# Kernel optimization log

Measured on AMD Instinct MI355X. Metric: run time of the kernel, lower is better.

The kernel has to match this reference:

```python
import jax, jax.numpy as jnp
import numpy as np

N = 200000      # total nodes
E = 800000      # directed edges
G = 4096        # graphs in batch
D_DRUG = 128
D_CELL = 954
HID = 128
OUT = 128
EPS = 1e-5      # BatchNorm eps


def _bn(x, gamma, beta):
    # training-mode BatchNorm1d (batch statistics, biased var), dropout is eval/identity
    m = jnp.mean(x, axis=0)
    v = jnp.mean((x - m) ** 2, axis=0)
    return gamma * (x - m) * jax.lax.rsqrt(v + EPS) + beta


def _gcn_conv(x, edge_index, W, b):
    # PyG GCNConv: add self-loops, symmetric normalization, aggregate, then bias
    src = jnp.concatenate([edge_index[0], jnp.arange(N)])
    dst = jnp.concatenate([edge_index[1], jnp.arange(N)])
    ones = jnp.ones(src.shape[0], dtype=x.dtype)
    deg = jax.ops.segment_sum(ones, dst, num_segments=N)
    dinv = jnp.where(deg > 0, jax.lax.rsqrt(jnp.maximum(deg, 1.0)), 0.0)
    norm = dinv[src] * dinv[dst]                      # [E+N]
    h = x @ W                                         # [N, out]
    msg = h[src] * norm[:, None]                      # gather + scale
    out = jax.ops.segment_sum(msg, dst, num_segments=N)  # scatter-add
    return out + b


def setup_inputs() -> dict:
    key = jax.random.key(0)
    ks = jax.random.split(key, 12)
    x = jax.random.normal(ks[0], (N, D_DRUG), jnp.float32)
    edge_index = jax.random.randint(ks[1], (2, E), 0, N)
    ibatch = (jnp.arange(N) * G) // N  # sorted, every graph non-empty
    gexpr = jax.random.normal(ks[2], (G, D_CELL), jnp.float32)

    def w(k, shape):
        return jax.random.normal(k, shape, jnp.float32) / np.float32(np.sqrt(shape[0]))

    return {
        "x": x, "edge_index": edge_index, "ibatch": ibatch, "gexpr": gexpr,
        "W1": w(ks[3], (D_DRUG, HID)), "b1": jnp.zeros((HID,), jnp.float32),
        "g1": jnp.ones((HID,), jnp.float32), "be1": jnp.zeros((HID,), jnp.float32),
        "W2": w(ks[4], (HID, OUT)), "b2": jnp.zeros((OUT,), jnp.float32),
        "g2": jnp.ones((OUT,), jnp.float32), "be2": jnp.zeros((OUT,), jnp.float32),
        "Wc1": w(ks[5], (D_CELL, HID)), "bc1": jnp.zeros((HID,), jnp.float32),
        "gc": jnp.ones((HID,), jnp.float32), "bec": jnp.zeros((HID,), jnp.float32),
        "Wc2": w(ks[6], (HID, OUT)), "bc2": jnp.zeros((OUT,), jnp.float32),
    }


def reference(x, edge_index, ibatch, gexpr,
              W1, b1, g1, be1, W2, b2, g2, be2,
              Wc1, bc1, gc, bec, Wc2, bc2):
    # drug branch
    h = _gcn_conv(x, edge_index, W1, b1)
    h = _bn(jax.nn.relu(h), g1, be1)
    h = _gcn_conv(h, edge_index, W2, b2)
    h = _bn(jax.nn.relu(h), g2, be2)
    x_drug = jax.ops.segment_max(h, ibatch, num_segments=G)  # global_max_pool
    # cellline branch
    c = jnp.tanh(gexpr @ Wc1 + bc1)
    c = _bn(c, gc, bec)
    x_cell = jax.nn.relu(c @ Wc2 + bc2)
    return x_drug, x_cell
```

## Files before the change

### kernel.cpp

```cpp
#include <hip/hip_runtime.h>

#define NFEAT 128

typedef __attribute__((ext_vector_type(4))) float f32x4;
typedef __attribute__((ext_vector_type(8))) short bf16x8;

__device__ __forceinline__ unsigned short f2bf(float f) {
    unsigned u = __builtin_bit_cast(unsigned, f);
    u += 0x7fffu + ((u >> 16) & 1u);
    return (unsigned short)(u >> 16);
}
__device__ __forceinline__ float bf2f(unsigned short s) {
    unsigned u = ((unsigned)s) << 16;
    return __builtin_bit_cast(float, u);
}

__device__ __forceinline__ void dma16(const void* g, void* l) {
    __builtin_amdgcn_global_load_lds(
        (const __attribute__((address_space(1))) unsigned int*)g,
        (__attribute__((address_space(3))) unsigned int*)l, 16, 0, 0);
}

template <int ACT, typename OutT, typename AT>
__global__ __launch_bounds__(256) void gemm_dma(
    const AT* __restrict__ A, const unsigned short* __restrict__ Bt,
    OutT* __restrict__ C, int M, int ldA, int ldB,
    const float* __restrict__ bias, const float* __restrict__ dscale)
{
    constexpr bool AF32 = (sizeof(AT) == 4);
    __shared__ AT ash[64 * 128];
    const int tid = threadIdx.x;
    const int wv = tid >> 6, lane = tid & 63;
    const int l16 = lane & 15, quad = lane >> 4;
    const int kbase = blockIdx.y * 128;
    const long tile0 = (long)blockIdx.x * 64;

    const int nc0 = (wv & 1) * 64;
    bf16x8 bfr[4][4];
#pragma unroll
    for (int nt = 0; nt < 4; ++nt) {
        const unsigned short* bp =
            Bt + (size_t)(nc0 + nt * 16 + l16) * ldB + kbase + quad * 8;
#pragma unroll
        for (int ks = 0; ks < 4; ++ks)
            bfr[nt][ks] = *(const bf16x8*)(bp + ks * 32);
    }

    {
        const int r0 = wv * 16;
        if constexpr (AF32) {
#pragma unroll
            for (int j = 0; j < 8; ++j) {
                const float* gp = (const float*)A +
                    (size_t)(tile0 + r0 + j * 2 + (lane >> 5)) * ldA + kbase +
                    (lane & 31) * 4;
                dma16(gp, (void*)&ash[(r0 + j * 2) * 128]);
            }
        } else {
#pragma unroll
            for (int j = 0; j < 4; ++j) {
                const unsigned short* gp = (const unsigned short*)A +
                    (size_t)(tile0 + r0 + j * 4 + (lane >> 4)) * ldA + kbase +
                    l16 * 8;
                dma16(gp, (void*)&ash[(r0 + j * 4) * 128]);
            }
        }
    }
    __syncthreads();

    const int rh = wv >> 1;
    bf16x8 af[2][4];
#pragma unroll
    for (int mt = 0; mt < 2; ++mt) {
        const int row = rh * 32 + mt * 16 + l16;
#pragma unroll
        for (int ks = 0; ks < 4; ++ks) {
            if constexpr (AF32) {
                const float* lp = (const float*)&ash[0] + row * 128 + ks * 32 + quad * 8;
                f32x4 v0 = *(const f32x4*)lp;
                f32x4 v1 = *(const f32x4*)(lp + 4);
                bf16x8 t;
                t[0] = (short)f2bf(v0[0]); t[1] = (short)f2bf(v0[1]);
                t[2] = (short)f2bf(v0[2]); t[3] = (short)f2bf(v0[3]);
                t[4] = (short)f2bf(v1[0]); t[5] = (short)f2bf(v1[1]);
                t[6] = (short)f2bf(v1[2]); t[7] = (short)f2bf(v1[3]);
                af[mt][ks] = t;
            } else {
                af[mt][ks] = *(const bf16x8*)((const unsigned short*)&ash[0] +
                                              row * 128 + ks * 32 + quad * 8);
            }
        }
    }

    f32x4 acc[2][4];
#pragma unroll
    for (int a = 0; a < 2; ++a)
#pragma unroll
        for (int b = 0; b < 4; ++b) acc[a][b] = (f32x4){0.f, 0.f, 0.f, 0.f};
#pragma unroll
    for (int ks = 0; ks < 4; ++ks)
#pragma unroll
        for (int nt = 0; nt < 4; ++nt)
#pragma unroll
            for (int mt = 0; mt < 2; ++mt)
                acc[mt][nt] = __builtin_amdgcn_mfma_f32_16x16x32_bf16(
                    af[mt][ks], bfr[nt][ks], acc[mt][nt], 0, 0, 0);

    C += (size_t)blockIdx.y * M * NFEAT;
    float ds[2][4];
#pragma unroll
    for (int mt = 0; mt < 2; ++mt)
#pragma unroll
        for (int r = 0; r < 4; ++r) {
            long row = tile0 + rh * 32 + mt * 16 + quad * 4 + r;
            ds[mt][r] = dscale ? dscale[row] : 1.f;
        }
#pragma unroll
    for (int nt = 0; nt < 4; ++nt) {
        int col = nc0 + nt * 16 + l16;
        float bv = bias ? bias[col] : 0.f;
#pragma unroll
        for (int mt = 0; mt < 2; ++mt) {
            long rbase = tile0 + rh * 32 + mt * 16 + quad * 4;
#pragma unroll
            for (int r = 0; r < 4; ++r) {
                float v = acc[mt][nt][r] + bv;
                if (ACT == 1) v = tanhf(v);
                if (ACT == 2) v = fmaxf(v, 0.f);
                v *= ds[mt][r];
                if constexpr (sizeof(OutT) == 2)
                    C[(size_t)(rbase + r) * NFEAT + col] = (OutT)f2bf(v);
                else
                    C[(size_t)(rbase + r) * NFEAT + col] = (OutT)v;
            }
        }
    }
}

__global__ void k_transpose(const float* __restrict__ W, unsigned short* __restrict__ Wt,
                            int K, int Kp)
{
    int idx = blockIdx.x * 256 + threadIdx.x;
    if (idx >= 128 * Kp) return;
    int n = idx / Kp, k = idx - n * Kp;
    Wt[idx] = (k < K) ? f2bf(W[(size_t)k * NFEAT + n]) : (unsigned short)0;
}

__global__ void k_bnfold_w(const float* __restrict__ sums8, const float* __restrict__ gamma,
                           const float* __restrict__ beta, float invN,
                           const float* __restrict__ W, const float* __restrict__ extra,
                           unsigned short* __restrict__ Wt, float* __restrict__ brow)
{
    __shared__ float ssc[128], ssh[128];
    int t = threadIdx.x;
    if (t < 128) {
        float s = 0.f, s2 = 0.f;
#pragma unroll
        for (int c = 0; c < 8; ++c) { s += sums8[c * 256 + t]; s2 += sums8[c * 256 + 128 + t]; }
        float mean = s * invN;
        float var = s2 * invN - mean * mean;
        float rstd = rsqrtf(fmaxf(var, 0.f) + 1e-5f);
        float sc = gamma[t] * rstd;
        ssc[t] = sc;
        ssh[t] = beta[t] - mean * sc;
    }
    __syncthreads();
    if (blockIdx.x < 64) {
        int idx = blockIdx.x * 256 + t;
        int n = idx >> 7, k = idx & 127;
        Wt[idx] = f2bf(W[(size_t)k * NFEAT + n] * ssc[k]);
    } else if (t < 128) {
        float s = extra ? extra[t] : 0.f;
        for (int k = 0; k < 128; ++k) s += ssh[k] * W[(size_t)k * NFEAT + t];
        brow[t] = s;
    }
}

__global__ void k_finalize8(const float* __restrict__ sums8, const float* __restrict__ gamma,
                            const float* __restrict__ beta, float* __restrict__ scale,
                            float* __restrict__ shift, float invN)
{
    int j = threadIdx.x;
    float s = 0.f, s2 = 0.f;
#pragma unroll
    for (int c = 0; c < 8; ++c) { s += sums8[c * 256 + j]; s2 += sums8[c * 256 + 128 + j]; }
    float mean = s * invN;
    float var = s2 * invN - mean * mean;
    float rstd = rsqrtf(fmaxf(var, 0.f) + 1e-5f);
    float sc = gamma[j] * rstd;
    scale[j] = sc;
    shift[j] = beta[j] - mean * sc;
}

__global__ void k_padA(const float* __restrict__ g, float* __restrict__ Ap,
                       int G, int DC, int DCP)
{
    long idx = (long)blockIdx.x * 256 + threadIdx.x;
    if (idx >= (long)G * DCP) return;
    long i = idx / DCP; int k = (int)(idx - i * DCP);
    Ap[idx] = (k < DC) ? g[i * DC + k] : 0.f;
}

__global__ void k_degi(const int* __restrict__ dst, int* __restrict__ deg, int E)
{
    int e = blockIdx.x * 256 + threadIdx.x;
    if (e < E) atomicAdd(&deg[dst[e]], 1);
}

__global__ __launch_bounds__(256) void k_scan1(const int* __restrict__ deg,
        int* __restrict__ rowptr, int* __restrict__ bsum, float* __restrict__ dinv, int N)
{
    __shared__ int sh[256];
    int t = threadIdx.x;
    int base = blockIdx.x * 1024 + t * 4;
    int v[4];
#pragma unroll
    for (int j = 0; j < 4; ++j) {
        v[j] = (base + j < N) ? deg[base + j] : 0;
        if (base + j < N) dinv[base + j] = rsqrtf((float)(v[j] + 1));
    }
    int s = v[0] + v[1] + v[2] + v[3];
    sh[t] = s;
    __syncthreads();
    int incl = s;
    for (int off = 1; off < 256; off <<= 1) {
        int x = (t >= off) ? sh[t - off] : 0;
        __syncthreads();
        incl += x;
        sh[t] = incl;
        __syncthreads();
    }
    int run = incl - s;
#pragma unroll
    for (int j = 0; j < 4; ++j) {
        if (base + j < N) rowptr[base + j] = run;
        run += v[j];
    }
    if (t == 255) bsum[blockIdx.x] = incl;
}

__global__ void k_scan2(int* __restrict__ bsum, int nb)
{
    __shared__ int sh[256];
    int t = threadIdx.x;
    int s = (t < nb) ? bsum[t] : 0;
    sh[t] = s;
    __syncthreads();
    int incl = s;
    for (int off = 1; off < 256; off <<= 1) {
        int x = (t >= off) ? sh[t - off] : 0;
        __syncthreads();
        incl += x;
        sh[t] = incl;
        __syncthreads();
    }
    if (t < nb) bsum[t] = incl - s;
}

__global__ void k_scan3(int* __restrict__ rowptr, int* __restrict__ cursor,
                        const int* __restrict__ bsum, int N, int E)
{
    int i = blockIdx.x * 256 + threadIdx.x;
    if (i < N) {
        int v = rowptr[i] + bsum[i >> 10];
        rowptr[i] = v;
        cursor[i] = v;
    } else if (i == N) {
        rowptr[N] = E;
    }
}

__global__ void k_fill(const int* __restrict__ src, const int* __restrict__ dst,
                       int* __restrict__ cursor, int* __restrict__ csr, int E)
{
    int e = blockIdx.x * 256 + threadIdx.x;
    if (e < E) {
        int pos = atomicAdd(&cursor[dst[e]], 1);
        csr[pos] = src[e];
    }
}

__device__ __forceinline__ void unpack_add(float* acc, uint4 a)
{
    acc[0] += bf2f((unsigned short)(a.x & 0xffff));
    acc[1] += bf2f((unsigned short)(a.x >> 16));
    acc[2] += bf2f((unsigned short)(a.y & 0xffff));
    acc[3] += bf2f((unsigned short)(a.y >> 16));
    acc[4] += bf2f((unsigned short)(a.z & 0xffff));
    acc[5] += bf2f((unsigned short)(a.z >> 16));
    acc[6] += bf2f((unsigned short)(a.w & 0xffff));
    acc[7] += bf2f((unsigned short)(a.w >> 16));
}

__device__ __forceinline__ void row_gather(const unsigned short* __restrict__ h,
    const int* __restrict__ rowptr, const int* __restrict__ csr,
    long i, int f, int N, float* acc)
{
    int lo = rowptr[i], hi = rowptr[i + 1];
    int n = hi - lo;
    int idx[6];
#pragma unroll
    for (int j = 0; j < 6; ++j) {
        int cv = csr[lo + j];
        idx[j] = (j < n) ? cv : N;
    }
    uint4 ga[6];
#pragma unroll
    for (int j = 0; j < 6; ++j)
        ga[j] = *(const uint4*)(h + ((size_t)idx[j] << 7) + f);
    uint4 gs = *(const uint4*)(h + ((size_t)i << 7) + f);
#pragma unroll
    for (int j = 0; j < 6; ++j) unpack_add(acc, ga[j]);
    unpack_add(acc, gs);
    if (n > 6) {
        int e = lo + 6;
        for (; e + 1 < hi; e += 2) {
            uint4 a = *(const uint4*)(h + ((size_t)csr[e] << 7) + f);
            uint4 b = *(const uint4*)(h + ((size_t)csr[e + 1] << 7) + f);
            unpack_add(acc, a); unpack_add(acc, b);
        }
        if (e < hi) {
            uint4 a = *(const uint4*)(h + ((size_t)csr[e] << 7) + f);
            unpack_add(acc, a);
        }
    }
}

__global__ __launch_bounds__(256, 6) void k_agg(
    const unsigned short* __restrict__ h, const int* __restrict__ rowptr,
    const int* __restrict__ csr, const float* __restrict__ dinv,
    const float* __restrict__ bias, unsigned short* __restrict__ out,
    float* __restrict__ sums8, int N)
{
    __shared__ float red[4][256];
    const int tid = threadIdx.x;
    const int wv = tid >> 6, lane = tid & 63;
    const int f = (tid & 15) << 3;
    const long g0 = (long)blockIdx.x * 16 + (tid >> 4);
    const long gstride = (long)gridDim.x * 16;

    f32x4 b0 = *(const f32x4*)&bias[f];
    f32x4 b1 = *(const f32x4*)&bias[f + 4];

    float s8[8], q8[8];
#pragma unroll
    for (int j = 0; j < 8; ++j) { s8[j] = 0.f; q8[j] = 0.f; }

    for (long i = g0; i < N; i += gstride) {
        float acc[8];
#pragma unroll
        for (int j = 0; j < 8; ++j) acc[j] = 0.f;
        row_gather(h, rowptr, csr, i, f, N, acc);

        float di = dinv[i];
        unsigned short o[8];
#pragma unroll
        for (int j = 0; j < 8; ++j) {
            float bj = (j < 4) ? b0[j] : b1[j - 4];
            float v = fmaxf(di * acc[j] + bj, 0.f);
            o[j] = f2bf(v);
            s8[j] += v; q8[j] += v * v;
        }
        *(uint4*)(out + (i << 7) + f) = *(const uint4*)o;
    }

#pragma unroll
    for (int j = 0; j < 8; ++j) {
        s8[j] += __shfl_xor(s8[j], 16);
        s8[j] += __shfl_xor(s8[j], 32);
        q8[j] += __shfl_xor(q8[j], 16);
        q8[j] += __shfl_xor(q8[j], 32);
    }
    if (lane < 16) {
#pragma unroll
        for (int j = 0; j < 8; ++j) {
            red[wv][f + j] = s8[j];
            red[wv][128 + f + j] = q8[j];
        }
    }
    __syncthreads();
    float tot = red[0][tid] + red[1][tid] + red[2][tid] + red[3][tid];
    atomicAdd(&sums8[(blockIdx.x & 7) * 256 + tid], tot);
}

__global__ __launch_bounds__(256, 6) void k_aggmax(
    const unsigned short* __restrict__ h, const int* __restrict__ rowptr,
    const int* __restrict__ csr, const float* __restrict__ dinv,
    const float* __restrict__ bias, int* __restrict__ gmax, int* __restrict__ gmin,
    float* __restrict__ sums8, int N, int G, int NB)
{
    __shared__ float red[4][256];
    __shared__ int lmax[3][128], lmin[3][128];
    const int tid = threadIdx.x;
    const int wv = tid >> 6, lane = tid & 63;
    const int f = (tid & 15) << 3;
    const int grp = tid >> 4;
    const int b = blockIdx.x;
    const int g_lo = (int)(((long long)b * G) / NB);
    const int g_hi = (int)(((long long)(b + 1) * G) / NB);
    const int ngr = g_hi - g_lo;
    const int rstart = (int)(((long long)g_lo * N + G - 1) / G);
    const int rend   = (int)(((long long)g_hi * N + G - 1) / G);
    const int bnd1   = (int)(((long long)(g_lo + 1) * N + G - 1) / G);
    const int bnd2   = (ngr >= 3) ? (int)(((long long)(g_lo + 2) * N + G - 1) / G)
                                  : rend;

    for (int idx = tid; idx < 3 * 128; idx += 256) {
        ((int*)lmax)[idx] = 0;
        ((int*)lmin)[idx] = 0x7f800000;
    }
    __syncthreads();

    f32x4 b0 = *(const f32x4*)&bias[f];
    f32x4 b1 = *(const f32x4*)&bias[f + 4];

    float s8[8], q8[8];
#pragma unroll
    for (int j = 0; j < 8; ++j) { s8[j] = 0.f; q8[j] = 0.f; }

    for (long i = rstart + grp; i < rend; i += 16) {
        float acc[8];
#pragma unroll
        for (int j = 0; j < 8; ++j) acc[j] = 0.f;
        row_gather(h, rowptr, csr, i, f, N, acc);

        float di = dinv[i];
        int gi = (i >= bnd1) + (i >= bnd2);
        int* lmx = &lmax[gi][f];
        int* lmn = &lmin[gi][f];
#pragma unroll
        for (int j = 0; j < 8; ++j) {
            float bj = (j < 4) ? b0[j] : b1[j - 4];
            float v = fmaxf(di * acc[j] + bj, 0.f);
            s8[j] += v; q8[j] += v * v;
            int bits = __builtin_bit_cast(int, v);
            atomicMax(&lmx[j], bits);
            atomicMin(&lmn[j], bits);
        }
    }

#pragma unroll
    for (int j = 0; j < 8; ++j) {
        s8[j] += __shfl_xor(s8[j], 16);
        s8[j] += __shfl_xor(s8[j], 32);
        q8[j] += __shfl_xor(q8[j], 16);
        q8[j] += __shfl_xor(q8[j], 32);
    }
    if (lane < 16) {
#pragma unroll
        for (int j = 0; j < 8; ++j) {
            red[wv][f + j] = s8[j];
            red[wv][128 + f + j] = q8[j];
        }
    }
    __syncthreads();
    float tot = red[0][tid] + red[1][tid] + red[2][tid] + red[3][tid];
    atomicAdd(&sums8[(blockIdx.x & 7) * 256 + tid], tot);

    for (int idx = tid; idx < ngr * 128; idx += 256) {
        int gg = idx >> 7, j = idx & 127;
        gmax[(size_t)(g_lo + gg) * 128 + j] = lmax[gg][j];
        gmin[(size_t)(g_lo + gg) * 128 + j] = lmin[gg][j];
    }
}

__global__ void k_segapply(const int* __restrict__ gmax, const int* __restrict__ gmin,
                           const float* __restrict__ scale, const float* __restrict__ shift,
                           float* __restrict__ out, int total)
{
    int idx = blockIdx.x * 256 + threadIdx.x;
    if (idx >= total) return;
    int j = idx & 127;
    float sc = scale[j], sh = shift[j];
    int bits = (sc >= 0.f) ? gmax[idx] : gmin[idx];
    out[idx] = sc * __builtin_bit_cast(float, bits) + sh;
}

__global__ void k_cellred(const float* __restrict__ p, const float* __restrict__ bias,
                          unsigned short* __restrict__ cbuf, float* __restrict__ sums8, int G)
{
    int j = threadIdx.x & 127;
    int slot = blockIdx.x * 2 + (threadIdx.x >> 7);
    int nslots = gridDim.x * 2;
    const size_t st = (size_t)G * NFEAT;
    float b = bias[j], s = 0.f, s2 = 0.f;
    for (int i = slot; i < G; i += nslots) {
        size_t o = (size_t)i * NFEAT + j;
        float v = b;
#pragma unroll
        for (int c = 0; c < 8; ++c) v += p[o + c * st];
        v = tanhf(v);
        cbuf[o] = f2bf(v);
        s += v; s2 += v * v;
    }
    atomicAdd(&sums8[(blockIdx.x & 7) * 256 + j], s);
    atomicAdd(&sums8[(blockIdx.x & 7) * 256 + 128 + j], s2);
}

extern "C" void kernel_launch(void* const* d_in, const int* in_sizes, int n_in,
                              void* d_out, int out_size, void* d_ws, size_t ws_size,
                              hipStream_t stream)
{
    const float* x     = (const float*)d_in[0];
    const int*   ei    = (const int*)d_in[1];
    const float* gexpr = (const float*)d_in[3];
    const float* W1  = (const float*)d_in[4];
    const float* b1  = (const float*)d_in[5];
    const float* g1  = (const float*)d_in[6];
    const float* be1 = (const float*)d_in[7];
    const float* W2  = (const float*)d_in[8];
    const float* b2  = (const float*)d_in[9];
    const float* g2  = (const float*)d_in[10];
    const float* be2 = (const float*)d_in[11];
    const float* Wc1 = (const float*)d_in[12];
    const float* bc1 = (const float*)d_in[13];
    const float* gc  = (const float*)d_in[14];
    const float* bec = (const float*)d_in[15];
    const float* Wc2 = (const float*)d_in[16];
    const float* bc2 = (const float*)d_in[17];

    const int N = in_sizes[0] / NFEAT;
    const int E = in_sizes[1] / 2;
    const int G = in_sizes[3] / 954;
    const int DC = 954, DCP = 1024;

    char* wsp = (char*)d_ws;
    size_t off = 0;
    auto alloc = [&](size_t bytes) -> char* {
        char* p = wsp + off;
        off += (bytes + 255) & ~(size_t)255;
        return p;
    };
    unsigned short* agg    = (unsigned short*)alloc((size_t)N * NFEAT * 2);
    unsigned short* h      = (unsigned short*)alloc((size_t)(N + 1) * NFEAT * 2);
    float*          dinv   = (float*)alloc((size_t)N * 4);
    int*            deg    = (int*)alloc((size_t)N * 4);
    int*            rowptr = (int*)alloc((size_t)(N + 1) * 4);
    int*            cursor = (int*)alloc((size_t)N * 4);
    int*            csr    = (int*)alloc((size_t)(E + 8) * 4);
    int*            bsum   = (int*)alloc(256 * 4);
    float*          Apad   = (float*)alloc((size_t)G * DCP * 4);
    float*          pbuf   = (float*)alloc((size_t)8 * G * NFEAT * 4);
    unsigned short* cbuf   = (unsigned short*)alloc((size_t)G * NFEAT * 2);
    int*            gmax   = (int*)alloc((size_t)G * NFEAT * 4);
    int*            gmin   = (int*)alloc((size_t)G * NFEAT * 4);
    unsigned short* W1t    = (unsigned short*)alloc(128 * 128 * 2);
    unsigned short* W2t    = (unsigned short*)alloc(128 * 128 * 2);
    unsigned short* Wc1t   = (unsigned short*)alloc(128 * DCP * 2);
    unsigned short* Wc2t   = (unsigned short*)alloc(128 * 128 * 2);
    float*          stats  = (float*)alloc(8192 * 4);
    float* sums1 = stats,         * sums2 = stats + 2048, * sumsC = stats + 4096;
    float* scale2 = stats + 6144, * shift2 = stats + 6272;
    float* brow2  = stats + 6400, * browC  = stats + 6528;

    hipMemsetAsync(stats, 0, 6144 * 4, stream);
    hipMemsetAsync(deg, 0, (size_t)N * 4, stream);
    hipMemsetAsync(h + (size_t)N * NFEAT, 0, NFEAT * 2, stream);

    const int* esrc = ei;
    const int* edst = ei + E;

    k_transpose<<<(128 * 128 + 255) / 256, 256, 0, stream>>>(W1, W1t, 128, 128);
    k_transpose<<<(128 * DCP + 255) / 256, 256, 0, stream>>>(Wc1, Wc1t, DC, DCP);
    k_padA<<<(int)(((long)G * DCP + 255) / 256), 256, 0, stream>>>(gexpr, Apad, G, DC, DCP);

    const int nb = (N + 1023) / 1024;
    k_degi<<<(E + 255) / 256, 256, 0, stream>>>(edst, deg, E);
    k_scan1<<<nb, 256, 0, stream>>>(deg, rowptr, bsum, dinv, N);
    k_scan2<<<1, 256, 0, stream>>>(bsum, nb);
    k_scan3<<<(N + 1 + 255) / 256, 256, 0, stream>>>(rowptr, cursor, bsum, N, E);
    k_fill<<<(E + 255) / 256, 256, 0, stream>>>(esrc, edst, cursor, csr, E);

    const int gtiles = N / 64;
    const int ablocks = 1536;
    const int NB = 1536;

    gemm_dma<0, unsigned short, float><<<dim3(gtiles, 1), 256, 0, stream>>>(
        x, W1t, h, N, 128, 128, nullptr, dinv);
    k_agg<<<ablocks, 256, 0, stream>>>(h, rowptr, csr, dinv, b1, agg, sums1, N);

    k_bnfold_w<<<65, 256, 0, stream>>>(sums1, g1, be1, 1.f / (float)N, W2, nullptr, W2t, brow2);
    gemm_dma<0, unsigned short, unsigned short><<<dim3(gtiles, 1), 256, 0, stream>>>(
        agg, W2t, h, N, 128, 128, brow2, dinv);

    k_aggmax<<<NB, 256, 0, stream>>>(h, rowptr, csr, dinv, b2, gmax, gmin, sums2, N, G, NB);
    k_finalize8<<<1, 128, 0, stream>>>(sums2, g2, be2, scale2, shift2, 1.f / (float)N);

    float* outp = (float*)d_out;
    k_segapply<<<(G * NFEAT + 255) / 256, 256, 0, stream>>>(
        gmax, gmin, scale2, shift2, outp, G * NFEAT);

    gemm_dma<0, float, float><<<dim3(G / 64, 8), 256, 0, stream>>>(
        Apad, Wc1t, pbuf, G, DCP, DCP, nullptr, nullptr);
    k_cellred<<<32, 256, 0, stream>>>(pbuf, bc1, cbuf, sumsC, G);
    k_bnfold_w<<<65, 256, 0, stream>>>(sumsC, gc, bec, 1.f / (float)G, Wc2, bc2, Wc2t, browC);
    gemm_dma<2, float, unsigned short><<<dim3(G / 64, 1), 256, 0, stream>>>(
        cbuf, Wc2t, outp + (size_t)G * NFEAT, G, 128, 128, browC, nullptr);
}
```

Before: 539.0 us.

## Simplify neighbor gather loop and keep per-graph max/min in registers

Replaces the fixed 6-wide padded speculative gather with a plain 4-way unrolled CSR loop and drops the dummy zero row. k_aggmax now processes exactly two graphs per block and accumulates max/min in registers, flushing to LDS atomics only at graph boundaries. The agg grid grows and the occupancy hint in launch_bounds is removed. Fewer LDS atomics, but less memory-level parallelism in the gather for short rows.

```diff
diff --git a/kernel.cpp b/kernel.cpp
--- a/kernel.cpp
+++ b/kernel.cpp
@@ -294,39 +294,29 @@
 
 __device__ __forceinline__ void row_gather(const unsigned short* __restrict__ h,
     const int* __restrict__ rowptr, const int* __restrict__ csr,
-    long i, int f, int N, float* acc)
+    long i, int f, float* acc)
 {
     int lo = rowptr[i], hi = rowptr[i + 1];
-    int n = hi - lo;
-    int idx[6];
-#pragma unroll
-    for (int j = 0; j < 6; ++j) {
-        int cv = csr[lo + j];
-        idx[j] = (j < n) ? cv : N;
-    }
-    uint4 ga[6];
-#pragma unroll
-    for (int j = 0; j < 6; ++j)
-        ga[j] = *(const uint4*)(h + ((size_t)idx[j] << 7) + f);
-    uint4 gs = *(const uint4*)(h + ((size_t)i << 7) + f);
-#pragma unroll
-    for (int j = 0; j < 6; ++j) unpack_add(acc, ga[j]);
-    unpack_add(acc, gs);
-    if (n > 6) {
-        int e = lo + 6;
-        for (; e + 1 < hi; e += 2) {
-            uint4 a = *(const uint4*)(h + ((size_t)csr[e] << 7) + f);
-            uint4 b = *(const uint4*)(h + ((size_t)csr[e + 1] << 7) + f);
-            unpack_add(acc, a); unpack_add(acc, b);
-        }
-        if (e < hi) {
-            uint4 a = *(const uint4*)(h + ((size_t)csr[e] << 7) + f);
-            unpack_add(acc, a);
-        }
-    }
-}
-
-__global__ __launch_bounds__(256, 6) void k_agg(
+    int e = lo;
+    for (; e + 3 < hi; e += 4) {
+        int s0 = csr[e], s1 = csr[e + 1], s2 = csr[e + 2], s3 = csr[e + 3];
+        uint4 a = *(const uint4*)(h + ((size_t)s0 << 7) + f);
+        uint4 b = *(const uint4*)(h + ((size_t)s1 << 7) + f);
+        uint4 c = *(const uint4*)(h + ((size_t)s2 << 7) + f);
+        uint4 d = *(const uint4*)(h + ((size_t)s3 << 7) + f);
+        unpack_add(acc, a); unpack_add(acc, b);
+        unpack_add(acc, c); unpack_add(acc, d);
+    }
+    for (; e < hi; ++e) {
+        int s0 = csr[e];
+        uint4 a = *(const uint4*)(h + ((size_t)s0 << 7) + f);
+        unpack_add(acc, a);
+    }
+    uint4 hs = *(const uint4*)(h + ((size_t)i << 7) + f);
+    unpack_add(acc, hs);
+}
+
+__global__ __launch_bounds__(256) void k_agg(
     const unsigned short* __restrict__ h, const int* __restrict__ rowptr,
     const int* __restrict__ csr, const float* __restrict__ dinv,
     const float* __restrict__ bias, unsigned short* __restrict__ out,
@@ -350,7 +340,7 @@
         float acc[8];
 #pragma unroll
         for (int j = 0; j < 8; ++j) acc[j] = 0.f;
-        row_gather(h, rowptr, csr, i, f, N, acc);
+        row_gather(h, rowptr, csr, i, f, acc);
 
         float di = dinv[i];
         unsigned short o[8];
@@ -383,29 +373,24 @@
     atomicAdd(&sums8[(blockIdx.x & 7) * 256 + tid], tot);
 }
 
-__global__ __launch_bounds__(256, 6) void k_aggmax(
+__global__ __launch_bounds__(256) void k_aggmax(
     const unsigned short* __restrict__ h, const int* __restrict__ rowptr,
     const int* __restrict__ csr, const float* __restrict__ dinv,
     const float* __restrict__ bias, int* __restrict__ gmax, int* __restrict__ gmin,
-    float* __restrict__ sums8, int N, int G, int NB)
+    float* __restrict__ sums8, int N, int G)
 {
     __shared__ float red[4][256];
-    __shared__ int lmax[3][128], lmin[3][128];
+    __shared__ int lmax[2][128], lmin[2][128];
     const int tid = threadIdx.x;
     const int wv = tid >> 6, lane = tid & 63;
     const int f = (tid & 15) << 3;
     const int grp = tid >> 4;
-    const int b = blockIdx.x;
-    const int g_lo = (int)(((long long)b * G) / NB);
-    const int g_hi = (int)(((long long)(b + 1) * G) / NB);
-    const int ngr = g_hi - g_lo;
+    const int g_lo = blockIdx.x * 2;
     const int rstart = (int)(((long long)g_lo * N + G - 1) / G);
-    const int rend   = (int)(((long long)g_hi * N + G - 1) / G);
+    const int rend   = (int)(((long long)(g_lo + 2) * N + G - 1) / G);
     const int bnd1   = (int)(((long long)(g_lo + 1) * N + G - 1) / G);
-    const int bnd2   = (ngr >= 3) ? (int)(((long long)(g_lo + 2) * N + G - 1) / G)
-                                  : rend;
-
-    for (int idx = tid; idx < 3 * 128; idx += 256) {
+
+    for (int idx = tid; idx < 2 * 128; idx += 256) {
         ((int*)lmax)[idx] = 0;
         ((int*)lmin)[idx] = 0x7f800000;
     }
@@ -414,29 +399,44 @@
     f32x4 b0 = *(const f32x4*)&bias[f];
     f32x4 b1 = *(const f32x4*)&bias[f + 4];
 
-    float s8[8], q8[8];
-#pragma unroll
-    for (int j = 0; j < 8; ++j) { s8[j] = 0.f; q8[j] = 0.f; }
+    float s8[8], q8[8], rmx[8], rmn[8];
+#pragma unroll
+    for (int j = 0; j < 8; ++j) {
+        s8[j] = 0.f; q8[j] = 0.f;
+        rmx[j] = 0.f; rmn[j] = __builtin_bit_cast(float, 0x7f800000);
+    }
+    int cur = 0;
 
     for (long i = rstart + grp; i < rend; i += 16) {
         float acc[8];
 #pragma unroll
         for (int j = 0; j < 8; ++j) acc[j] = 0.f;
-        row_gather(h, rowptr, csr, i, f, N, acc);
+        row_gather(h, rowptr, csr, i, f, acc);
 
         float di = dinv[i];
-        int gi = (i >= bnd1) + (i >= bnd2);
-        int* lmx = &lmax[gi][f];
-        int* lmn = &lmin[gi][f];
+        int gi = (i >= bnd1);
+        if (gi != cur) {
+#pragma unroll
+            for (int j = 0; j < 8; ++j) {
+                atomicMax(&lmax[cur][f + j], __builtin_bit_cast(int, rmx[j]));
+                atomicMin(&lmin[cur][f + j], __builtin_bit_cast(int, rmn[j]));
+                rmx[j] = 0.f; rmn[j] = __builtin_bit_cast(float, 0x7f800000);
+            }
+            cur = gi;
+        }
 #pragma unroll
         for (int j = 0; j < 8; ++j) {
             float bj = (j < 4) ? b0[j] : b1[j - 4];
             float v = fmaxf(di * acc[j] + bj, 0.f);
             s8[j] += v; q8[j] += v * v;
-            int bits = __builtin_bit_cast(int, v);
-            atomicMax(&lmx[j], bits);
-            atomicMin(&lmn[j], bits);
-        }
+            rmx[j] = fmaxf(rmx[j], v);
+            rmn[j] = fminf(rmn[j], v);
+        }
+    }
+#pragma unroll
+    for (int j = 0; j < 8; ++j) {
+        atomicMax(&lmax[cur][f + j], __builtin_bit_cast(int, rmx[j]));
+        atomicMin(&lmin[cur][f + j], __builtin_bit_cast(int, rmn[j]));
     }
 
 #pragma unroll
@@ -457,7 +457,7 @@
     float tot = red[0][tid] + red[1][tid] + red[2][tid] + red[3][tid];
     atomicAdd(&sums8[(blockIdx.x & 7) * 256 + tid], tot);
 
-    for (int idx = tid; idx < ngr * 128; idx += 256) {
+    for (int idx = tid; idx < 2 * 128; idx += 256) {
         int gg = idx >> 7, j = idx & 127;
         gmax[(size_t)(g_lo + gg) * 128 + j] = lmax[gg][j];
         gmin[(size_t)(g_lo + gg) * 128 + j] = lmin[gg][j];
@@ -532,12 +532,12 @@
         return p;
     };
     unsigned short* agg    = (unsigned short*)alloc((size_t)N * NFEAT * 2);
-    unsigned short* h      = (unsigned short*)alloc((size_t)(N + 1) * NFEAT * 2);
+    unsigned short* h      = (unsigned short*)alloc((size_t)N * NFEAT * 2);
     float*          dinv   = (float*)alloc((size_t)N * 4);
     int*            deg    = (int*)alloc((size_t)N * 4);
     int*            rowptr = (int*)alloc((size_t)(N + 1) * 4);
     int*            cursor = (int*)alloc((size_t)N * 4);
-    int*            csr    = (int*)alloc((size_t)(E + 8) * 4);
+    int*            csr    = (int*)alloc((size_t)E * 4);
     int*            bsum   = (int*)alloc(256 * 4);
     float*          Apad   = (float*)alloc((size_t)G * DCP * 4);
     float*          pbuf   = (float*)alloc((size_t)8 * G * NFEAT * 4);
@@ -555,7 +555,6 @@
 
     hipMemsetAsync(stats, 0, 6144 * 4, stream);
     hipMemsetAsync(deg, 0, (size_t)N * 4, stream);
-    hipMemsetAsync(h + (size_t)N * NFEAT, 0, NFEAT * 2, stream);
 
     const int* esrc = ei;
     const int* edst = ei + E;
@@ -572,8 +571,7 @@
     k_fill<<<(E + 255) / 256, 256, 0, stream>>>(esrc, edst, cursor, csr, E);
 
     const int gtiles = N / 64;
-    const int ablocks = 1536;
-    const int NB = 1536;
+    const int ablocks = 2048;
 
     gemm_dma<0, unsigned short, float><<<dim3(gtiles, 1), 256, 0, stream>>>(
         x, W1t, h, N, 128, 128, nullptr, dinv);
@@ -583,7 +581,7 @@
     gemm_dma<0, unsigned short, unsigned short><<<dim3(gtiles, 1), 256, 0, stream>>>(
         agg, W2t, h, N, 128, 128, brow2, dinv);
 
-    k_aggmax<<<NB, 256, 0, stream>>>(h, rowptr, csr, dinv, b2, gmax, gmin, sums2, N, G, NB);
+    k_aggmax<<<G / 2, 256, 0, stream>>>(h, rowptr, csr, dinv, b2, gmax, gmin, sums2, N, G);
     k_finalize8<<<1, 128, 0, stream>>>(sums2, g2, be2, scale2, shift2, 1.f / (float)N);
 
     float* outp = (float*)d_out;
```

New measurement: 515.3 us. 4.4% less time.
